# Performance work log

Measured on AMD Instinct MI355X. Metric: run time of the kernel, lower is better.

## Reference

```python
import jax, jax.numpy as jnp
import numpy as np

B, S, DIN, D = 8, 1024, 512, 512


def _xavier(key, fan_in, fan_out):
    bound = float(np.sqrt(6.0 / (fan_in + fan_out)))
    return jax.random.uniform(key, (fan_in, fan_out), jnp.float32, -bound, bound)


def setup_inputs() -> dict:
    key = jax.random.key(0)
    ks = jax.random.split(key, 6)
    return {
        'x': jax.random.normal(ks[0], (B, S, DIN), jnp.float32),
        # weights stored as [in, out] (transpose of torch Linear.weight); biases zero-init per _init_weights
        'W_in': _xavier(ks[1], DIN, 4 * D), 'b_in': jnp.zeros((4 * D,), jnp.float32),
        'W_ig': _xavier(ks[2], D, D), 'b_ig': jnp.zeros((D,), jnp.float32),
        'W_fg': _xavier(ks[3], D, D), 'b_fg': jnp.zeros((D,), jnp.float32),
        'W_og': _xavier(ks[4], D, D), 'b_og': jnp.zeros((D,), jnp.float32),
        'W_out': _xavier(ks[5], D, D), 'b_out': jnp.zeros((D,), jnp.float32),
    }


def reference(x, W_in, b_in, W_ig, b_ig, W_fg, b_fg, W_og, b_og, W_out, b_out):
    b, s, _ = x.shape
    d = W_ig.shape[0]
    proj = x @ W_in + b_in                      # [B,S,4D]
    q, k, v, _g = jnp.split(proj, 4, axis=-1)   # g (silu branch) is unused in the original loop
    q = jnp.tanh(q)
    k = jnp.tanh(k)
    # dropout is identity in eval mode
    i_g = jax.nn.sigmoid(v @ W_ig + b_ig)       # per-step gates are pointwise linears -> batch them
    f_g = jax.nn.sigmoid(v @ W_fg + b_fg)
    o_g = jax.nn.sigmoid(v @ W_og + b_og)

    def step(carry, ts):
        C, n = carry                            # C: [B,D,D], n: [B,D]
        qt, kt, vt, it, ft, ot = ts             # each [B,D]
        C = ft[:, :, None] * C + it[:, :, None] * (kt[:, :, None] * vt[:, None, :])
        n = ft * n + it * kt
        h_cand = jnp.einsum('bd,bde->be', qt, C)
        denom = jnp.maximum(jnp.sum(qt * n, axis=-1, keepdims=True), 1e-6)
        h = ot * h_cand / denom
        return (C, n), h

    tm = lambda a: jnp.swapaxes(a, 0, 1)        # time-major for scan
    C0 = jnp.zeros((b, d, d), x.dtype)
    n0 = jnp.zeros((b, d), x.dtype)
    (Cf, nf), hs = jax.lax.scan(step, (C0, n0), (tm(q), tm(k), tm(v), tm(i_g), tm(f_g), tm(o_g)))
    hs = jnp.swapaxes(hs, 0, 1)                 # [B,S,D]
    out = hs @ W_out + b_out
    return out, Cf, nf, hs[:, -1, :]
```

## Files before the change

kernel.cpp:

```cpp
#include <hip/hip_runtime.h>

#define S_ 1024
#define D_ 512
#define DCH 8
#define NDCH 128
#define CT 32
#define NCT 32

using bf16x8 = __attribute__((ext_vector_type(8))) short;
using f32x4  = __attribute__((ext_vector_type(4))) float;

__device__ __forceinline__ unsigned short f2bf(float x) {
    unsigned int u = __float_as_uint(x);
    u = (u + 0x7FFFu + ((u >> 16) & 1u)) >> 16;
    return (unsigned short)u;
}
__device__ __forceinline__ float bf2f(unsigned short s) {
    return __uint_as_float(((unsigned int)s) << 16);
}
__device__ __forceinline__ bf16x8 cvt8(const float* __restrict__ p) {
    float4 a = *(const float4*)p;
    float4 b = *(const float4*)(p + 4);
    bf16x8 r;
    r[0] = (short)f2bf(a.x); r[1] = (short)f2bf(a.y);
    r[2] = (short)f2bf(a.z); r[3] = (short)f2bf(a.w);
    r[4] = (short)f2bf(b.x); r[5] = (short)f2bf(b.y);
    r[6] = (short)f2bf(b.z); r[7] = (short)f2bf(b.w);
    return r;
}
__device__ __forceinline__ void gload_lds16(const void* g, void* l) {
    __builtin_amdgcn_global_load_lds(
        (const __attribute__((address_space(1))) void*)g,
        (__attribute__((address_space(3))) void*)l, 16, 0, 0);
}


__global__ __launch_bounds__(256)
void prep_w(const float* __restrict__ W_in, const float* __restrict__ W_ig,
            const float* __restrict__ W_fg, const float* __restrict__ W_og,
            const float* __restrict__ W_out,
            unsigned short* __restrict__ Wh, unsigned short* __restrict__ Wl)
{
    const int n    = blockIdx.x * 256 + threadIdx.x;
    const int kblk = blockIdx.y;

    const float* src; int ldw, col;
    if (n < 1536)       { src = W_in;  ldw = 2048; col = n; }
    else if (n < 3072)  {
        const int g = (n - 1536) >> 9;
        src = (g == 0) ? W_ig : (g == 1) ? W_fg : W_og;
        ldw = 512; col = (n - 1536) & 511;
    } else              { src = W_out; ldw = 512; col = n - 3072; }

    unsigned int hw[16], lw[16];
#pragma unroll
    for (int j = 0; j < 32; j += 2) {
        const int k = kblk * 32 + j;
        float f0 = src[(size_t)k * ldw + col];
        float f1 = src[(size_t)(k + 1) * ldw + col];
        unsigned short h0 = f2bf(f0), h1 = f2bf(f1);
        unsigned short l0 = f2bf(f0 - bf2f(h0)), l1 = f2bf(f1 - bf2f(h1));
        hw[j >> 1] = (unsigned int)h0 | ((unsigned int)h1 << 16);
        lw[j >> 1] = (unsigned int)l0 | ((unsigned int)l1 << 16);
    }
    const size_t base = ((size_t)(n >> 7) * 16 + kblk) * 4096 + ((n & 127) << 5);
    const int perm = n & 3;
#pragma unroll
    for (int g = 0; g < 4; ++g) {
        const size_t dst = base + (size_t)((g ^ perm) << 3);
        *(uint4*)(Wh + dst) = make_uint4(hw[g*4], hw[g*4+1], hw[g*4+2], hw[g*4+3]);
        *(uint4*)(Wl + dst) = make_uint4(lw[g*4], lw[g*4+1], lw[g*4+2], lw[g*4+3]);
    }
}

__global__ __launch_bounds__(256)
void cvt_a(const float* __restrict__ A, int lda,
           unsigned short* __restrict__ Ah, unsigned short* __restrict__ Al)
{
    const int m    = blockIdx.x * 256 + threadIdx.x;
    const int kblk = blockIdx.y;
    const float* p = A + (size_t)m * lda + kblk * 32;
    const size_t base = ((size_t)(m >> 7) * 16 + kblk) * 4096 + ((m & 127) << 5);
    const int perm = m & 3;
#pragma unroll
    for (int g = 0; g < 4; ++g) {
        float4 a = *(const float4*)(p + g * 8);
        float4 b = *(const float4*)(p + g * 8 + 4);
        float f[8] = {a.x, a.y, a.z, a.w, b.x, b.y, b.z, b.w};
        unsigned int hw[4], lw[4];
#pragma unroll
        for (int j = 0; j < 4; ++j) {
            unsigned short h0 = f2bf(f[2*j]), h1 = f2bf(f[2*j+1]);
            unsigned short l0 = f2bf(f[2*j] - bf2f(h0));
            unsigned short l1 = f2bf(f[2*j+1] - bf2f(h1));
            hw[j] = (unsigned int)h0 | ((unsigned int)h1 << 16);
            lw[j] = (unsigned int)l0 | ((unsigned int)l1 << 16);
        }
        const size_t dst = base + (size_t)((g ^ perm) << 3);
        *(uint4*)(Ah + dst) = make_uint4(hw[0], hw[1], hw[2], hw[3]);
        *(uint4*)(Al + dst) = make_uint4(lw[0], lw[1], lw[2], lw[3]);
    }
}

template<int MODE>
__global__ __launch_bounds__(256)
void gemm_mfma(const unsigned short* __restrict__ Ah,
               const unsigned short* __restrict__ Al,
               const unsigned short* __restrict__ Wh,
               const unsigned short* __restrict__ Wl,
               const float* __restrict__ qkv,
               const float* __restrict__ bb0, const float* __restrict__ bb1,
               const float* __restrict__ bb2,
               float* __restrict__ Co, int ldc)
{
    __shared__ unsigned short lds[2][4][4096];

    const int tid  = threadIdx.x;
    const int lane = tid & 63;
    const int wv   = tid >> 6;
    const int nbt  = (MODE == 2) ? 4 : 12;
    const int cpx  = gridDim.x >> 3;
    const int swz  = (blockIdx.x & 7) * cpx + (blockIdx.x >> 3);
    const int n0blk = swz % nbt;
    const int m0blk = swz / nbt;
    const int l15  = lane & 15;
    const int kg   = lane >> 4;
    const int nbase = (MODE == 0) ? 0 : (MODE == 1) ? 1536 : 3072;

    const size_t abase = (size_t)m0blk * 16 * 4096;
    const size_t wbase = (size_t)((nbase >> 7) + n0blk) * 16 * 4096;

    f32x4 acc[4][4];
#pragma unroll
    for (int mf = 0; mf < 4; ++mf)
#pragma unroll
        for (int nf = 0; nf < 4; ++nf) acc[mf][nf] = (f32x4){0.f, 0.f, 0.f, 0.f};

    auto STAGE = [&](int buf, int kblk) {
        const unsigned short* srcs[4] = {
            Ah + abase + (size_t)kblk * 4096, Al + abase + (size_t)kblk * 4096,
            Wh + wbase + (size_t)kblk * 4096, Wl + wbase + (size_t)kblk * 4096};
#pragma unroll
        for (int p = 0; p < 4; ++p)
#pragma unroll
            for (int h = 0; h < 2; ++h)
                gload_lds16(srcs[p] + h * 2048 + (size_t)tid * 8,
                            &lds[buf][p][h * 2048 + wv * 512]);
    };

    STAGE(0, 0);
    __syncthreads();

    int cur = 0;
    for (int ks = 0; ks < 16; ++ks) {
        if (ks + 1 < 16) STAGE(cur ^ 1, ks + 1);

        bf16x8 ah[4], al[4], bh[4], bl[4];
#pragma unroll
        for (int i = 0; i < 4; ++i) {
            const int ra = (wv >> 1) * 64 + i * 16 + l15;
            const int oa = ra * 32 + ((kg ^ (ra & 3)) << 3);
            ah[i] = *(const bf16x8*)&lds[cur][0][oa];
            al[i] = *(const bf16x8*)&lds[cur][1][oa];
            const int rw = (wv & 1) * 64 + i * 16 + l15;
            const int ow = rw * 32 + ((kg ^ (rw & 3)) << 3);
            bh[i] = *(const bf16x8*)&lds[cur][2][ow];
            bl[i] = *(const bf16x8*)&lds[cur][3][ow];
        }
#pragma unroll
        for (int nf = 0; nf < 4; ++nf)
#pragma unroll
            for (int mf = 0; mf < 4; ++mf) {
                acc[mf][nf] = __builtin_amdgcn_mfma_f32_16x16x32_bf16(ah[mf], bh[nf], acc[mf][nf], 0, 0, 0);
                acc[mf][nf] = __builtin_amdgcn_mfma_f32_16x16x32_bf16(al[mf], bh[nf], acc[mf][nf], 0, 0, 0);
                acc[mf][nf] = __builtin_amdgcn_mfma_f32_16x16x32_bf16(ah[mf], bl[nf], acc[mf][nf], 0, 0, 0);
            }
        __syncthreads();
        cur ^= 1;
    }

    const int m0 = m0blk * 128 + (wv >> 1) * 64;
    const int n0 = n0blk * 128 + (wv & 1) * 64;
#pragma unroll
    for (int mf = 0; mf < 4; ++mf) {
#pragma unroll
        for (int vi = 0; vi < 4; ++vi) {
            const int m = m0 + mf * 16 + kg * 4 + vi;
            float* crow = Co + (size_t)m * ldc;
#pragma unroll
            for (int nf = 0; nf < 4; ++nf) {
                const int n = n0 + nf * 16 + l15;
                float bias;
                if (MODE == 1) {
                    const int g = n >> 9;
                    bias = (g == 0 ? bb0 : g == 1 ? bb1 : bb2)[n & 511];
                } else {
                    bias = bb0[n];
                }
                float v = acc[mf][nf][vi] + bias;
                if (MODE == 0) {
                    if (n < 1024) v = tanhf(v);
                } else if (MODE == 1) {
                    v = 1.0f / (1.0f + expf(-v));
                    if (n < 512) v *= qkv[(size_t)m * 1536 + 512 + n];
                }
                crow[n] = v;
            }
        }
    }
}

__global__ __launch_bounds__(512)
void nscan_local(const float* __restrict__ GG,
                 double* __restrict__ nend, double* __restrict__ Dend)
{
    const int b = blockIdx.x >> 7;
    const int c = blockIdx.x & 127;
    const int d = threadIdx.x;
    const float* gb = GG + (size_t)b * S_ * 1536 + (size_t)c * DCH * 1536;
    double n = 0.0, P = 1.0;
    for (int u = 0; u < DCH; ++u) {
        const float* row = gb + (size_t)u * 1536;
        const double ik = (double)row[d];
        const double f  = (double)row[512 + d];
        n = fma(f, n, ik);
        P *= f;
    }
    nend[(size_t)blockIdx.x * 512 + d] = n;
    Dend[(size_t)blockIdx.x * 512 + d] = P;
}

__global__ __launch_bounds__(512)
void nscan_stitch(const double* __restrict__ nend, const double* __restrict__ Dend,
                  double* __restrict__ n0a, float* __restrict__ nfO)
{
    const int b = blockIdx.x;
    const int d = threadIdx.x;
    double n0 = 0.0;
    for (int c = 0; c < NDCH; ++c) {
        const size_t idx = ((size_t)(b * NDCH + c)) * 512 + d;
        n0a[idx] = n0;
        n0 = fma(Dend[idx], n0, nend[idx]);
    }
    nfO[(size_t)b * 512 + d] = (float)n0;
}

__global__ __launch_bounds__(256)
void denom_kernel(const float* __restrict__ QKV, const float* __restrict__ GG,
                  const double* __restrict__ n0a, float* __restrict__ invd)
{
    const int lane = threadIdx.x & 63;
    const int widx = blockIdx.x * 4 + (threadIdx.x >> 6);
    const int b    = widx >> 7;
    const int c    = widx & 127;
    const int d0   = 4 * lane;

    const float* qb = QKV + (size_t)b * S_ * 1536 + (size_t)c * DCH * 1536;
    const float* gb = GG  + (size_t)b * S_ * 1536 + (size_t)c * DCH * 1536;
    const double* sp = n0a + (size_t)widx * 512;

    double n[2][4];
#pragma unroll
    for (int r = 0; r < 2; ++r) {
        double2 a = *(const double2*)(sp + d0 + 256 * r);
        double2 bb = *(const double2*)(sp + d0 + 256 * r + 2);
        n[r][0] = a.x; n[r][1] = a.y; n[r][2] = bb.x; n[r][3] = bb.y;
    }

    for (int t0 = 0; t0 < DCH; t0 += 4) {
        double dq[4];
#pragma unroll
        for (int i = 0; i < 4; ++i) {
            const float* qr = qb + (size_t)(t0 + i) * 1536;
            const float* gr = gb + (size_t)(t0 + i) * 1536;
            double acc = 0.0;
#pragma unroll
            for (int r = 0; r < 2; ++r) {
                float4 qf = *(const float4*)(qr + d0 + 256 * r);
                float4 kf = *(const float4*)(gr + d0 + 256 * r);
                float4 ff = *(const float4*)(gr + 512 + d0 + 256 * r);
                const float* qp = (const float*)&qf;
                const float* kp = (const float*)&kf;
                const float* fp = (const float*)&ff;
#pragma unroll
                for (int j = 0; j < 4; ++j) {
                    n[r][j] = fma((double)fp[j], n[r][j], (double)kp[j]);
                    acc = fma((double)qp[j], n[r][j], acc);
                }
            }
            dq[i] = acc;
        }
        double u0 = dq[0] + __shfl_xor(dq[0], 32);
        double u1 = dq[1] + __shfl_xor(dq[1], 32);
        double u2 = dq[2] + __shfl_xor(dq[2], 32);
        double u3 = dq[3] + __shfl_xor(dq[3], 32);
        double w0 = (lane & 32) ? u2 : u0;
        double w1 = (lane & 32) ? u3 : u1;
        w0 += __shfl_xor(w0, 16);
        w1 += __shfl_xor(w1, 16);
        double y = (lane & 16) ? w1 : w0;
        y += __shfl_xor(y, 8); y += __shfl_xor(y, 4);
        y += __shfl_xor(y, 2); y += __shfl_xor(y, 1);
        if ((lane & 15) == 0) {
            const int g = lane >> 4;
            const double den = (y > 1e-6) ? y : 1e-6;
            invd[(size_t)b * S_ + c * DCH + t0 + g] = (float)(1.0 / den);
        }
    }
}

__global__ __launch_bounds__(512)
void chunk_prep(float* __restrict__ qkv, float* __restrict__ gg)
{
    const int b = blockIdx.x >> 5;
    const int c = blockIdx.x & 31;
    const int d = threadIdx.x;
    float* qr = qkv + ((size_t)(b * S_ + c * CT)) * 1536 + d;
    float* gr = gg  + ((size_t)(b * S_ + c * CT)) * 1536 + d;
    float* ft = gr + 512;
    float F = 1.f;
    for (int u = 0; u < CT; ++u) {
        const float q = qr[0], ik = gr[0], f = gr[512];
        F *= f;
        qr[0] = q * F;
        gr[0] = ik / F;
        qr += 1536; gr += 1536;
    }
    ft[0] = F;
}

__global__ __launch_bounds__(256)
void chunk_A(const float* __restrict__ qkv, const float* __restrict__ gg,
             float* __restrict__ h1out)
{
    const int b   = blockIdx.x >> 5;
    const int c   = blockIdx.x & 31;
    const int tid = threadIdx.x;
    const int t   = tid & 31;
    const int g   = tid >> 5;

    __shared__ float sA[32][33];

    const size_t rb = (size_t)(b * S_ + c * CT);
    const float* qr = qkv + (rb + t) * 1536;
    const float* kb = gg + rb * 1536;

    {
        const int s0 = g * 4;
        const float* k0 = kb + (size_t)(s0 + 0) * 1536;
        const float* k1 = kb + (size_t)(s0 + 1) * 1536;
        const float* k2 = kb + (size_t)(s0 + 2) * 1536;
        const float* k3 = kb + (size_t)(s0 + 3) * 1536;
        float a0 = 0.f, a1 = 0.f, a2 = 0.f, a3 = 0.f;
        for (int d4 = 0; d4 < 512; d4 += 4) {
            float4 qv = *(const float4*)(qr + d4);
            float4 x0 = *(const float4*)(k0 + d4);
            float4 x1 = *(const float4*)(k1 + d4);
            float4 x2 = *(const float4*)(k2 + d4);
            float4 x3 = *(const float4*)(k3 + d4);
            a0 = fmaf(qv.x, x0.x, a0); a0 = fmaf(qv.y, x0.y, a0);
            a0 = fmaf(qv.z, x0.z, a0); a0 = fmaf(qv.w, x0.w, a0);
            a1 = fmaf(qv.x, x1.x, a1); a1 = fmaf(qv.y, x1.y, a1);
            a1 = fmaf(qv.z, x1.z, a1); a1 = fmaf(qv.w, x1.w, a1);
            a2 = fmaf(qv.x, x2.x, a2); a2 = fmaf(qv.y, x2.y, a2);
            a2 = fmaf(qv.z, x2.z, a2); a2 = fmaf(qv.w, x2.w, a2);
            a3 = fmaf(qv.x, x3.x, a3); a3 = fmaf(qv.y, x3.y, a3);
            a3 = fmaf(qv.z, x3.z, a3); a3 = fmaf(qv.w, x3.w, a3);
        }
        sA[t][s0 + 0] = (s0 + 0 <= t) ? a0 : 0.f;
        sA[t][s0 + 1] = (s0 + 1 <= t) ? a1 : 0.f;
        sA[t][s0 + 2] = (s0 + 2 <= t) ? a2 : 0.f;
        sA[t][s0 + 3] = (s0 + 3 <= t) ? a3 : 0.f;
    }
    __syncthreads();

    {
        const int e0 = g * 64;
        float4 h[16];
#pragma unroll
        for (int m = 0; m < 16; ++m) h[m] = make_float4(0.f, 0.f, 0.f, 0.f);
        const float* vb = qkv + rb * 1536 + 1024 + e0;
        for (int s = 0; s < CT; ++s) {
            const float a = sA[t][s];
            const float* vr = vb + (size_t)s * 1536;
#pragma unroll
            for (int m = 0; m < 16; ++m) {
                float4 vv = *(const float4*)(vr + m * 4);
                h[m].x = fmaf(a, vv.x, h[m].x);
                h[m].y = fmaf(a, vv.y, h[m].y);
                h[m].z = fmaf(a, vv.z, h[m].z);
                h[m].w = fmaf(a, vv.w, h[m].w);
            }
        }
        float* orow = h1out + (rb + t) * 512 + e0;
#pragma unroll
        for (int m = 0; m < 16; ++m) *(float4*)(orow + m * 4) = h[m];
    }
}

__global__ __launch_bounds__(512)
void chunk_cacc(const float* __restrict__ qkv, const float* __restrict__ gg,
                unsigned short* __restrict__ snap, int c0)
{
    const int b   = blockIdx.x;
    const int lc  = blockIdx.y;
    const int dq  = blockIdx.z;
    const int c   = c0 + lc;
    const int tid = threadIdx.x;
    const int te  = tid >> 4;
    const int td  = tid & 15;
    const int d0  = dq * 128 + td * 8;

    const size_t rb = (size_t)(b * S_ + c * CT);
    const size_t sb = ((size_t)lc * 8 + b) * 512;

    for (int p = 0; p < 2; ++p) {
        const int e0 = p * 256 + te * 8;
        float acc[8][8];
#pragma unroll
        for (int i = 0; i < 8; ++i)
#pragma unroll
            for (int j = 0; j < 8; ++j) acc[i][j] = 0.f;

#pragma unroll 4
        for (int u = 0; u < CT; ++u) {
            const float* vrow = qkv + (rb + u) * 1536 + 1024 + e0;
            const float* krow = gg  + (rb + u) * 1536 + d0;
            float4 v0 = *(const float4*)(vrow);
            float4 v1 = *(const float4*)(vrow + 4);
            float4 k0 = *(const float4*)(krow);
            float4 k1 = *(const float4*)(krow + 4);
            float ve[8] = {v0.x, v0.y, v0.z, v0.w, v1.x, v1.y, v1.z, v1.w};
            float kd[8] = {k0.x, k0.y, k0.z, k0.w, k1.x, k1.y, k1.z, k1.w};
#pragma unroll
            for (int i = 0; i < 8; ++i)
#pragma unroll
                for (int j = 0; j < 8; ++j)
                    acc[i][j] = fmaf(ve[i], kd[j], acc[i][j]);
        }

#pragma unroll
        for (int i = 0; i < 8; ++i) {
            uint4 pk;
            pk.x = (unsigned int)f2bf(acc[i][0]) | ((unsigned int)f2bf(acc[i][1]) << 16);
            pk.y = (unsigned int)f2bf(acc[i][2]) | ((unsigned int)f2bf(acc[i][3]) << 16);
            pk.z = (unsigned int)f2bf(acc[i][4]) | ((unsigned int)f2bf(acc[i][5]) << 16);
            pk.w = (unsigned int)f2bf(acc[i][6]) | ((unsigned int)f2bf(acc[i][7]) << 16);
            *(uint4*)(snap + (sb + e0 + i) * 512 + d0) = pk;
        }
    }
}

__global__ __launch_bounds__(256)
void chunk_cscan(const float* __restrict__ gg,
                 unsigned short* __restrict__ snap, float* __restrict__ Cst,
                 float* __restrict__ CfO, int c0, int nc)
{
    const int tid  = threadIdx.x;
    const int lane = tid & 63;
    const int wv   = tid >> 6;
    const int b    = blockIdx.x;
    const int eg   = blockIdx.y;
    const int dh   = blockIdx.z;
    const int ew   = eg * 16 + wv * 4;
    const int d0   = dh * 256 + 4 * lane;

    const float* gb = gg + (size_t)b * S_ * 1536;

    float C[4][4];
    if (c0 == 0) {
#pragma unroll
        for (int i = 0; i < 4; ++i)
#pragma unroll
            for (int j = 0; j < 4; ++j) C[i][j] = 0.f;
    } else {
#pragma unroll
        for (int j = 0; j < 4; ++j) {
            float4 cv = *(const float4*)&Cst[((size_t)b * 512 + d0 + j) * 512 + ew];
            C[0][j] = cv.x; C[1][j] = cv.y; C[2][j] = cv.z; C[3][j] = cv.w;
        }
    }

    ushort4 A0[4]; float4 F0;
    {
        const size_t sb = ((size_t)0 * 8 + b) * 512;
#pragma unroll
        for (int i = 0; i < 4; ++i)
            A0[i] = *(const ushort4*)(snap + (sb + ew + i) * 512 + d0);
        F0 = *(const float4*)(gb + (size_t)(c0 * CT) * 1536 + 512 + d0);
    }

    for (int lc = 0; lc < nc; ++lc) {
        ushort4 A1[4]; float4 F1;
        if (lc + 1 < nc) {
            const size_t sb = ((size_t)(lc + 1) * 8 + b) * 512;
#pragma unroll
            for (int i = 0; i < 4; ++i)
                A1[i] = *(const ushort4*)(snap + (sb + ew + i) * 512 + d0);
            F1 = *(const float4*)(gb + (size_t)((c0 + lc + 1) * CT) * 1536 + 512 + d0);
        }

        const int c = c0 + lc;
        if (c > 0) {
            const size_t sb = ((size_t)lc * 8 + b) * 512;
#pragma unroll
            for (int i = 0; i < 4; ++i) {
                uint2 pk;
                pk.x = (unsigned int)f2bf(C[i][0]) | ((unsigned int)f2bf(C[i][1]) << 16);
                pk.y = (unsigned int)f2bf(C[i][2]) | ((unsigned int)f2bf(C[i][3]) << 16);
                *(uint2*)(snap + (sb + ew + i) * 512 + d0) = pk;
            }
        }

        const float* fp = (const float*)&F0;
#pragma unroll
        for (int i = 0; i < 4; ++i) {
            C[i][0] = fp[0] * (C[i][0] + bf2f(A0[i].x));
            C[i][1] = fp[1] * (C[i][1] + bf2f(A0[i].y));
            C[i][2] = fp[2] * (C[i][2] + bf2f(A0[i].z));
            C[i][3] = fp[3] * (C[i][3] + bf2f(A0[i].w));
        }

        if (lc + 1 < nc) {
#pragma unroll
            for (int i = 0; i < 4; ++i) A0[i] = A1[i];
            F0 = F1;
        }
    }

    float* outp = (c0 + nc == NCT) ? CfO : Cst;
#pragma unroll
    for (int j = 0; j < 4; ++j)
        *(float4*)&outp[((size_t)b * 512 + d0 + j) * 512 + ew] =
            make_float4(C[0][j], C[1][j], C[2][j], C[3][j]);
}

__global__ __launch_bounds__(256)
void chunk_h2(const float* __restrict__ qkv, const float* __restrict__ gg,
              const unsigned short* __restrict__ snap,
              const float* __restrict__ invd,
              float* __restrict__ hs, float* __restrict__ hlO, int c0)
{
    const int eh   = blockIdx.x;
    const int lc   = blockIdx.y;
    const int b    = blockIdx.z;
    const int c    = c0 + lc;
    const int tid  = threadIdx.x;
    const int lane = tid & 63;
    const int wv   = tid >> 6;
    const int n0   = eh * 256 + wv * 64;
    const int l15  = lane & 15;
    const int kg   = lane >> 4;

    const size_t rb = (size_t)(b * S_ + c * CT);

    f32x4 acc[2][4];
#pragma unroll
    for (int mf = 0; mf < 2; ++mf)
#pragma unroll
        for (int nf = 0; nf < 4; ++nf) acc[mf][nf] = (f32x4){0.f, 0.f, 0.f, 0.f};

    if (c > 0) {
        const unsigned short* cb = snap + ((size_t)(lc * 8 + b) * 512) * 512;
        const float* q0p = qkv + (rb + l15) * 1536;
        const float* q1p = qkv + (rb + 16 + l15) * 1536;
#pragma unroll 4
        for (int k0 = 0; k0 < 512; k0 += 32) {
            const int kb = k0 + kg * 8;
            bf16x8 a0 = cvt8(q0p + kb);
            bf16x8 a1 = cvt8(q1p + kb);
#pragma unroll
            for (int nf = 0; nf < 4; ++nf) {
                const unsigned short* bp = cb + (size_t)(n0 + nf * 16 + l15) * 512 + kb;
                bf16x8 bf = *(const bf16x8*)bp;
                acc[0][nf] = __builtin_amdgcn_mfma_f32_16x16x32_bf16(a0, bf, acc[0][nf], 0, 0, 0);
                acc[1][nf] = __builtin_amdgcn_mfma_f32_16x16x32_bf16(a1, bf, acc[1][nf], 0, 0, 0);
            }
        }
    }

    const float* ivp = invd + (size_t)b * S_ + c * CT;
#pragma unroll
    for (int mf = 0; mf < 2; ++mf) {
#pragma unroll
        for (int vi = 0; vi < 4; ++vi) {
            const int tl  = mf * 16 + kg * 4 + vi;
            const float ivt = ivp[tl];
            float* hrow       = hs + (rb + tl) * 512;
            const float* orow = gg + (rb + tl) * 1536 + 1024;
            const bool last = (c * CT + tl == S_ - 1);
#pragma unroll
            for (int nf = 0; nf < 4; ++nf) {
                const int e  = n0 + nf * 16 + l15;
                const float h1 = hrow[e];
                const float ov = orow[e];
                const float r  = (acc[mf][nf][vi] + h1) * ov * ivt;
                hrow[e] = r;
                if (last) hlO[(size_t)b * 512 + e] = r;
            }
        }
    }
}

extern "C" void kernel_launch(void* const* d_in, const int* in_sizes, int n_in,
                              void* d_out, int out_size, void* d_ws, size_t ws_size,
                              hipStream_t stream)
{
    const float* x    = (const float*)d_in[0];
    const float* W_in = (const float*)d_in[1];
    const float* b_in = (const float*)d_in[2];
    const float* W_ig = (const float*)d_in[3];
    const float* b_ig = (const float*)d_in[4];
    const float* W_fg = (const float*)d_in[5];
    const float* b_fg = (const float*)d_in[6];
    const float* W_og = (const float*)d_in[7];
    const float* b_og = (const float*)d_in[8];
    const float* W_out= (const float*)d_in[9];
    const float* b_out= (const float*)d_in[10];

    float* out   = (float*)d_out;
    float* CfO   = out + (size_t)8 * 1024 * 512;
    float* nfO   = CfO + (size_t)8 * 512 * 512;
    float* hlO   = nfO + (size_t)8 * 512;

    float* qkv = (float*)d_ws;
    float* gg  = qkv + (size_t)8192 * 1536;
    float* hsb = gg  + (size_t)8192 * 1536;
    double* nend = (double*)hsb;
    double* Dend = nend + (size_t)8 * NDCH * 512;
    double* n0a  = Dend + (size_t)8 * NDCH * 512;
    float*  invd = hsb + (size_t)8192 * 512;
    float*  Cst  = invd + 8192;
    unsigned short* Wh = (unsigned short*)(Cst + (size_t)8 * 512 * 512);
    unsigned short* Wl = Wh + (size_t)3584 * 512;
    unsigned short* snap = Wl + (size_t)3584 * 512;

    const size_t WSB   = (size_t)((char*)snap - (char*)d_ws);
    const size_t SNAPC = (size_t)8 * 512 * 512 * 2;
    int nc; unsigned short* Ah;
    if (ws_size >= WSB + 32 * SNAPC)      { nc = 32; Ah = snap; }
    else if (ws_size >= WSB + 8 * SNAPC)  { nc = 8;  Ah = snap; }
    else                                  { nc = 2;  Ah = snap + 2 * (SNAPC / 2); }
    unsigned short* Al = Ah + (size_t)8192 * 512;

    prep_w<<<dim3(14, 16), 256, 0, stream>>>(W_in, W_ig, W_fg, W_og, W_out, Wh, Wl);
    cvt_a<<<dim3(32, 16), 256, 0, stream>>>(x, 512, Ah, Al);
    gemm_mfma<0><<<768, 256, 0, stream>>>(
        Ah, Al, Wh, Wl, qkv, b_in, b_in, b_in, qkv, 1536);
    cvt_a<<<dim3(32, 16), 256, 0, stream>>>(qkv + 1024, 1536, Ah, Al);
    gemm_mfma<1><<<768, 256, 0, stream>>>(
        Ah, Al, Wh, Wl, qkv, b_ig, b_fg, b_og, gg, 1536);
    nscan_local <<<1024, 512, 0, stream>>>(gg, nend, Dend);
    nscan_stitch<<<   8, 512, 0, stream>>>(nend, Dend, n0a, nfO);
    denom_kernel<<< 256, 256, 0, stream>>>(qkv, gg, n0a, invd);
    chunk_prep<<<256, 512, 0, stream>>>(qkv, gg);
    chunk_A<<<256, 256, 0, stream>>>(qkv, gg, hsb);
    for (int c0 = 0; c0 < NCT; c0 += nc) {
        chunk_cacc <<<dim3(8, nc, 4), 512, 0, stream>>>(qkv, gg, snap, c0);
        chunk_cscan<<<dim3(8, 32, 2), 256, 0, stream>>>(gg, snap, Cst, CfO, c0, nc);
        chunk_h2   <<<dim3(2, nc, 8), 256, 0, stream>>>(qkv, gg, snap, invd, hsb, hlO, c0);
    }
    cvt_a<<<dim3(32, 16), 256, 0, stream>>>(hsb, 512, Ah, Al);
    gemm_mfma<2><<<256, 256, 0, stream>>>(
        Ah, Al, Wh, Wl, qkv, b_out, b_out, b_out, out, 512);
}
```

Before: 462.9 us.

## Compute per-chunk V·Kᵀ outer-product sums with bf16 MFMA via LDS-transposed tiles

Rewrites chunk_cacc so the per-chunk sum of v⊗k outer products is computed with 16x16x32 bf16 MFMA instructions instead of scalar FP32 FMAs. V and K rows for the chunk are converted to bf16 and stored transposed in LDS (time along the contraction axis), then each wave computes a 64x128 output tile. Block size grows to 1024 threads and the grid halves in z. It trades FP32 accumulation of bf16-rounded inputs for matrix-core throughput, and uses narrow 2-byte scattered stores for the snapshot output.

Measured after the change: 406.4 us. -12.2%, faster.

```diff
diff --git a/kernel.cpp b/kernel.cpp
--- a/kernel.cpp
+++ b/kernel.cpp
@@ -33,7 +33,6 @@
         (const __attribute__((address_space(1))) void*)g,
         (__attribute__((address_space(3))) void*)l, 16, 0, 0);
 }
-
 
 __global__ __launch_bounds__(256)
 void prep_w(const float* __restrict__ W_in, const float* __restrict__ W_ig,
@@ -398,56 +397,92 @@
     }
 }
 
-__global__ __launch_bounds__(512)
+__global__ __launch_bounds__(1024)
 void chunk_cacc(const float* __restrict__ qkv, const float* __restrict__ gg,
                 unsigned short* __restrict__ snap, int c0)
 {
-    const int b   = blockIdx.x;
-    const int lc  = blockIdx.y;
-    const int dq  = blockIdx.z;
-    const int c   = c0 + lc;
-    const int tid = threadIdx.x;
-    const int te  = tid >> 4;
-    const int td  = tid & 15;
-    const int d0  = dq * 128 + td * 8;
+    __shared__ unsigned short vT[256][40];
+    __shared__ unsigned short kT[512][40];
+
+    const int b    = blockIdx.x;
+    const int lc   = blockIdx.y;
+    const int eh   = blockIdx.z;
+    const int c    = c0 + lc;
+    const int tid  = threadIdx.x;
+    const int lane = tid & 63;
+    const int wv   = tid >> 6;
+    const int l15  = lane & 15;
+    const int kg   = lane >> 4;
 
     const size_t rb = (size_t)(b * S_ + c * CT);
     const size_t sb = ((size_t)lc * 8 + b) * 512;
 
-    for (int p = 0; p < 2; ++p) {
-        const int e0 = p * 256 + te * 8;
-        float acc[8][8];
-#pragma unroll
-        for (int i = 0; i < 8; ++i)
-#pragma unroll
-            for (int j = 0; j < 8; ++j) acc[i][j] = 0.f;
-
-#pragma unroll 4
-        for (int u = 0; u < CT; ++u) {
-            const float* vrow = qkv + (rb + u) * 1536 + 1024 + e0;
-            const float* krow = gg  + (rb + u) * 1536 + d0;
-            float4 v0 = *(const float4*)(vrow);
-            float4 v1 = *(const float4*)(vrow + 4);
-            float4 k0 = *(const float4*)(krow);
-            float4 k1 = *(const float4*)(krow + 4);
-            float ve[8] = {v0.x, v0.y, v0.z, v0.w, v1.x, v1.y, v1.z, v1.w};
-            float kd[8] = {k0.x, k0.y, k0.z, k0.w, k1.x, k1.y, k1.z, k1.w};
-#pragma unroll
-            for (int i = 0; i < 8; ++i)
-#pragma unroll
-                for (int j = 0; j < 8; ++j)
-                    acc[i][j] = fmaf(ve[i], kd[j], acc[i][j]);
-        }
-
-#pragma unroll
-        for (int i = 0; i < 8; ++i) {
-            uint4 pk;
-            pk.x = (unsigned int)f2bf(acc[i][0]) | ((unsigned int)f2bf(acc[i][1]) << 16);
-            pk.y = (unsigned int)f2bf(acc[i][2]) | ((unsigned int)f2bf(acc[i][3]) << 16);
-            pk.z = (unsigned int)f2bf(acc[i][4]) | ((unsigned int)f2bf(acc[i][5]) << 16);
-            pk.w = (unsigned int)f2bf(acc[i][6]) | ((unsigned int)f2bf(acc[i][7]) << 16);
-            *(uint4*)(snap + (sb + e0 + i) * 512 + d0) = pk;
-        }
+    if (tid < 256) {
+        const float* vp = qkv + rb * 1536 + 1024 + eh * 256 + tid;
+        unsigned int pk[16];
+#pragma unroll
+        for (int u = 0; u < 32; u += 2) {
+            float f0 = vp[(size_t)u * 1536];
+            float f1 = vp[(size_t)(u + 1) * 1536];
+            pk[u >> 1] = (unsigned int)f2bf(f0) | ((unsigned int)f2bf(f1) << 16);
+        }
+        uint4* dst = (uint4*)&vT[tid][0];
+        dst[0] = make_uint4(pk[0],  pk[1],  pk[2],  pk[3]);
+        dst[1] = make_uint4(pk[4],  pk[5],  pk[6],  pk[7]);
+        dst[2] = make_uint4(pk[8],  pk[9],  pk[10], pk[11]);
+        dst[3] = make_uint4(pk[12], pk[13], pk[14], pk[15]);
+    } else if (tid < 768) {
+        const int d = tid - 256;
+        const float* kp = gg + rb * 1536 + d;
+        unsigned int pk[16];
+#pragma unroll
+        for (int u = 0; u < 32; u += 2) {
+            float f0 = kp[(size_t)u * 1536];
+            float f1 = kp[(size_t)(u + 1) * 1536];
+            pk[u >> 1] = (unsigned int)f2bf(f0) | ((unsigned int)f2bf(f1) << 16);
+        }
+        uint4* dst = (uint4*)&kT[d][0];
+        dst[0] = make_uint4(pk[0],  pk[1],  pk[2],  pk[3]);
+        dst[1] = make_uint4(pk[4],  pk[5],  pk[6],  pk[7]);
+        dst[2] = make_uint4(pk[8],  pk[9],  pk[10], pk[11]);
+        dst[3] = make_uint4(pk[12], pk[13], pk[14], pk[15]);
+    }
+    __syncthreads();
+
+    const int ebase = (wv & 3) * 64;
+    const int dbase = (wv >> 2) * 128;
+
+    bf16x8 a[4];
+#pragma unroll
+    for (int me = 0; me < 4; ++me)
+        a[me] = *(const bf16x8*)&vT[ebase + me * 16 + l15][kg * 8];
+
+#pragma unroll
+    for (int dp = 0; dp < 2; ++dp) {
+        f32x4 acc[4][4];
+#pragma unroll
+        for (int me = 0; me < 4; ++me)
+#pragma unroll
+            for (int nd = 0; nd < 4; ++nd) acc[me][nd] = (f32x4){0.f, 0.f, 0.f, 0.f};
+
+#pragma unroll
+        for (int nd = 0; nd < 4; ++nd) {
+            bf16x8 bfr = *(const bf16x8*)&kT[dbase + dp * 64 + nd * 16 + l15][kg * 8];
+#pragma unroll
+            for (int me = 0; me < 4; ++me)
+                acc[me][nd] = __builtin_amdgcn_mfma_f32_16x16x32_bf16(a[me], bfr, acc[me][nd], 0, 0, 0);
+        }
+
+#pragma unroll
+        for (int me = 0; me < 4; ++me)
+#pragma unroll
+            for (int vi = 0; vi < 4; ++vi) {
+                const int e = eh * 256 + ebase + me * 16 + kg * 4 + vi;
+                unsigned short* row = snap + (sb + e) * 512 + dbase + dp * 64;
+#pragma unroll
+                for (int nd = 0; nd < 4; ++nd)
+                    row[nd * 16 + l15] = f2bf(acc[me][nd][vi]);
+            }
     }
 }
 
@@ -656,7 +691,7 @@
     chunk_prep<<<256, 512, 0, stream>>>(qkv, gg);
     chunk_A<<<256, 256, 0, stream>>>(qkv, gg, hsb);
     for (int c0 = 0; c0 < NCT; c0 += nc) {
-        chunk_cacc <<<dim3(8, nc, 4), 512, 0, stream>>>(qkv, gg, snap, c0);
+        chunk_cacc <<<dim3(8, nc, 2), 1024, 0, stream>>>(qkv, gg, snap, c0);
         chunk_cscan<<<dim3(8, 32, 2), 256, 0, stream>>>(gg, snap, Cst, CfO, c0, nc);
         chunk_h2   <<<dim3(2, nc, 8), 256, 0, stream>>>(qkv, gg, snap, invd, hsb, hlO, c0);
     }
```
